# Kernel optimization log

Measured on AMD Instinct MI355X. Metric: run time of the kernel, lower is better.

The kernel has to match this reference:

```python
import jax, jax.numpy as jnp
import numpy as np

# Static configuration (matches init_kwargs / input_specs)
B, H, W, C = 16, 32, 32, 16
KH, KW = 3, 3
SH, SW = 1, 1
F = 32
HO = (H - KH) // SH + 1  # 30
WO = (W - KW) // SW + 1  # 30
K = KH * KW * C          # 144 window elements; +1 bias row -> 145
L = HO * WO              # 900 output positions per filter


def _gather_indices():
    # Faithful port of get_input_gather_indices (valid padding, non-vector input).
    row_off = np.arange(HO) * W * SH * C          # row offsets in flattened NHWC
    col_off = np.arange(WO) * SW * C              # col offsets
    offsets = (row_off[:, None] + col_off).reshape(-1)  # [L]
    ib = np.zeros((H, W, C))
    ib[:KH, :KW, :C] = 1
    iv = np.nonzero(ib.reshape(-1))[0]            # [K] flat indices of top-left window
    idx = iv[:, None] + offsets                   # [K, L]
    bias = np.full((1, L), H * W * C)             # bias row points at appended ones column
    return np.concatenate([idx, bias], 0).astype(np.int64)  # [K+1, L]

IDX = jnp.asarray(_gather_indices())


def setup_inputs() -> dict:
    key = jax.random.key(0)
    k1, k2 = jax.random.split(key)
    x = jax.random.normal(k1, (B, H, W, C), dtype=jnp.float32)
    # keras 'random_normal' initializer: mean 0, stddev 0.05
    flattened_weight = jax.random.normal(k2, (K + 1, 1, F), dtype=jnp.float32) * 0.05
    return {"x": x, "flattened_weight": flattened_weight}


def reference(x, flattened_weight):
    # flatten HWC, append bias ones column -> [B, H*W*C + 1]
    x_flat = x.reshape(B, -1)
    x_flat = jnp.concatenate([x_flat, jnp.ones((B, 1), x.dtype)], axis=-1)
    # gather window elements: [B, K+1, L]
    g = x_flat[:, IDX]
    # elementwise multiply with tiled weight [K+1,1,F] -> [B, K+1, L, F]
    y = g[..., None] * flattened_weight[None, :, :, :]
    # full_output_shape = [-1, K+1, Ho, Wo, F]
    return y.reshape(B, K + 1, HO, WO, F)
```

## Files before the change

kernel.cpp:

```cpp
#include <hip/hip_runtime.h>


#define BB   16
#define HH   32
#define WW   32
#define CC   16
#define FF   32
#define KP1  145
#define HOO  30
#define WOO  30
#define LL   900

__global__ __launch_bounds__(256) void vinput_conv_kernel(
    const float* __restrict__ x,
    const float* __restrict__ w,
    float* __restrict__ out,
    int total4)
{
    const int stride = gridDim.x * blockDim.x;
    for (int u = blockIdx.x * blockDim.x + threadIdx.x; u < total4; u += stride) {
        const int f4   = u & 7;
        const int rest = u >> 3;
        const int l    = rest % LL;
        const int bk   = rest / LL;
        const int k    = bk % KP1;
        const int b    = bk / KP1;

        float g;
        if (k == 144) {
            g = 1.0f;
        } else {
            const int kh = k / 48;
            const int r  = k - kh * 48;
            const int kw = r >> 4;
            const int c  = r & 15;
            const int ho = l / 30;
            const int wo = l - ho * 30;
            g = x[(((b * HH) + (ho + kh)) * WW + (wo + kw)) * CC + c];
        }

        const float4 wv = *reinterpret_cast<const float4*>(w + k * FF + f4 * 4);
        float4 o;
        o.x = g * wv.x;
        o.y = g * wv.y;
        o.z = g * wv.z;
        o.w = g * wv.w;
        reinterpret_cast<float4*>(out)[u] = o;
    }
}

extern "C" void kernel_launch(void* const* d_in, const int* in_sizes, int n_in,
                              void* d_out, int out_size, void* d_ws, size_t ws_size,
                              hipStream_t stream) {
    const float* x = (const float*)d_in[0];
    const float* w = (const float*)d_in[1];
    float* out = (float*)d_out;

    const int total4 = (BB * KP1 * LL * FF) / 4;

    const int block = 256;
    const int grid  = 2048;
    vinput_conv_kernel<<<grid, block, 0, stream>>>(x, w, out, total4);
}
```

Baseline: 48.81 us.

## Assign one block per (batch, k) row and use nontemporal stores

The grid-stride loop over flat indices is replaced by one block per (b,k) pair, so the weight vector and the k-decoding are computed once per thread instead of per element. Output writes use nontemporal stores to avoid polluting cache on a large write-only stream, and the bias row becomes a pure broadcast store. This removes per-element integer division and modulo work. The risk is that the nontemporal hint, or the 2320-block grid with a 7200-iteration row loop, changes write bandwidth behaviour.

```diff
diff --git a/kernel.cpp b/kernel.cpp
--- a/kernel.cpp
+++ b/kernel.cpp
@@ -7,45 +7,47 @@
 #define CC   16
 #define FF   32
 #define KP1  145
-#define HOO  30
-#define WOO  30
 #define LL   900
+#define ROW4 (LL * FF / 4)
+
+typedef float f32x4 __attribute__((ext_vector_type(4)));
 
 __global__ __launch_bounds__(256) void vinput_conv_kernel(
     const float* __restrict__ x,
     const float* __restrict__ w,
-    float* __restrict__ out,
-    int total4)
+    float* __restrict__ out)
 {
-    const int stride = gridDim.x * blockDim.x;
-    for (int u = blockIdx.x * blockDim.x + threadIdx.x; u < total4; u += stride) {
-        const int f4   = u & 7;
-        const int rest = u >> 3;
-        const int l    = rest % LL;
-        const int bk   = rest / LL;
-        const int k    = bk % KP1;
-        const int b    = bk / KP1;
+    const unsigned bid = blockIdx.x;
+    const unsigned b   = bid / KP1;
+    const unsigned k   = bid - b * KP1;
 
-        float g;
-        if (k == 144) {
-            g = 1.0f;
-        } else {
-            const int kh = k / 48;
-            const int r  = k - kh * 48;
-            const int kw = r >> 4;
-            const int c  = r & 15;
-            const int ho = l / 30;
-            const int wo = l - ho * 30;
-            g = x[(((b * HH) + (ho + kh)) * WW + (wo + kw)) * CC + c];
+    const unsigned tid = threadIdx.x;
+    const unsigned f4  = tid & 7;
+
+    const f32x4 wv = *reinterpret_cast<const f32x4*>(w + k * FF + f4 * 4);
+
+    f32x4* __restrict__ out4 = reinterpret_cast<f32x4*>(out) + (size_t)bid * ROW4;
+
+    if (k == 144) {
+        for (unsigned u = tid; u < ROW4; u += 256) {
+            __builtin_nontemporal_store(wv, out4 + u);
         }
+    } else {
+        const unsigned kh = k / 48;
+        const unsigned r  = k - kh * 48;
+        const unsigned kw = r >> 4;
+        const unsigned c  = r & 15;
+        const float* __restrict__ xbase =
+            x + ((b * HH + kh) * WW + kw) * CC + c;
 
-        const float4 wv = *reinterpret_cast<const float4*>(w + k * FF + f4 * 4);
-        float4 o;
-        o.x = g * wv.x;
-        o.y = g * wv.y;
-        o.z = g * wv.z;
-        o.w = g * wv.w;
-        reinterpret_cast<float4*>(out)[u] = o;
+        for (unsigned u = tid; u < ROW4; u += 256) {
+            const unsigned l  = u >> 3;
+            const unsigned ho = l / 30;
+            const unsigned wo = l - ho * 30;
+            const float g = xbase[ho * (WW * CC) + wo * CC];
+            f32x4 o = g * wv;
+            __builtin_nontemporal_store(o, out4 + u);
+        }
     }
 }
 
@@ -56,9 +58,6 @@
     const float* w = (const float*)d_in[1];
     float* out = (float*)d_out;
 
-    const int total4 = (BB * KP1 * LL * FF) / 4;
-
-    const int block = 256;
-    const int grid  = 2048;
-    vinput_conv_kernel<<<grid, block, 0, stream>>>(x, w, out, total4);
+    const int grid = BB * KP1;
+    vinput_conv_kernel<<<grid, 256, 0, stream>>>(x, w, out);
 }
```

Result: slower. 58.31 us (+19.5%).
